# Kernel tuning notes

Measured on AMD Instinct MI355X. Metric: run time of the kernel, lower is better.

## Reference

```python
import jax, jax.numpy as jnp
import numpy as np

HEADS, DIM_HEAD = 8, 64  # per init_kwargs


def cdist(x, w):
    """Euclidean distance between rows of x [..., n, d] and w [m, d] -> [..., n, m].
    Matches torch.cdist (non-squared) / L2DistanceLinear(squared=False)."""
    sq = (x * x).sum(-1, keepdims=True) + (w * w).sum(-1) - 2.0 * (x @ w.T)
    return jnp.sqrt(jnp.maximum(sq, 0.0))


def setup_inputs() -> dict:
    key = jax.random.key(0)
    k1, k2, k3 = jax.random.split(key, 3)
    B, N, D = 4, 2048, 512
    dim_inner = HEADS * DIM_HEAD  # 512
    x = jax.random.normal(k1, (B, N, D), dtype=jnp.float32)
    w_qkv = jax.random.normal(k2, (3 * dim_inner, D), dtype=jnp.float32)
    w_out = jax.random.normal(k3, (D, dim_inner), dtype=jnp.float32)
    return {"x": x, "w_qkv": w_qkv, "w_out": w_out}


def reference(x, w_qkv, w_out):
    B, N, D = x.shape
    scale = DIM_HEAD ** -0.5

    # L2-distance QKV projection (cdist, non-squared, no negate/bias)
    qkv = cdist(x, w_qkv)                                  # [B, N, 3*H*DH]
    qkv = qkv.reshape(B, N, 3, HEADS, DIM_HEAD).transpose(2, 0, 3, 1, 4)  # [3, B, H, N, DH]
    q, k, v = qkv[0], qkv[1], qkv[2]

    # neg squared-L2 attention scores: -(||q||^2 + ||k||^2 - 2 q.k)
    q_sq = (q * q).sum(-1)                                 # [B, H, N]
    k_sq = (k * k).sum(-1)                                 # [B, H, N]
    dots = jnp.einsum('bhid,bhjd->bhij', q, k)             # [B, H, N, N]
    sim = -(q_sq[..., :, None] + k_sq[..., None, :] - 2.0 * dots) * scale

    attn = jax.nn.softmax(sim, axis=-1)
    out = jnp.einsum('bhij,bhjd->bhid', attn, v)           # [B, H, N, DH]
    out = out.transpose(0, 2, 1, 3).reshape(B, N, HEADS * DIM_HEAD)

    # L2-distance output projection
    return cdist(out, w_out)                               # [B, N, D]
```

## Files before the change

### kernel.cpp

```cpp
#include <hip/hip_runtime.h>
#include <stdint.h>

typedef float v4f  __attribute__((ext_vector_type(4)));
typedef float v16f __attribute__((ext_vector_type(16)));
typedef short v8s  __attribute__((ext_vector_type(8)));
typedef uint32_t u32;

#define DEVI static __device__ __forceinline__

DEVI unsigned short f2bf(float f) {
    u32 u = __builtin_bit_cast(u32, f);
    u = (u + 0x7fffu + ((u >> 16) & 1u)) >> 16;
    return (unsigned short)u;
}
DEVI float bf2f(unsigned short h) {
    u32 u = ((u32)h) << 16;
    return __builtin_bit_cast(float, u);
}

template <typename T>
DEVI void async16(const T* g, T* l) {
    __builtin_amdgcn_global_load_lds(
        (const __attribute__((address_space(1))) u32*)g,
        (__attribute__((address_space(3))) u32*)l, 16, 0, 0);
}

DEVI v4f bmfma(v8s a, v8s b, v4f c) {
    return __builtin_amdgcn_mfma_f32_16x16x32_bf16(a, b, c, 0, 0, 0);
}
DEVI v16f bmfma32(v8s a, v8s b, v16f c) {
    return __builtin_amdgcn_mfma_f32_32x32x16_bf16(a, b, c, 0, 0, 0);
}

#if __has_builtin(__builtin_amdgcn_permlane32_swap)
#define HAVE_PLSWAP 1
typedef unsigned int v2u __attribute__((ext_vector_type(2)));
#endif

DEVI void swap32(u32 a, u32 b, u32& lo, u32& hi) {
#ifdef HAVE_PLSWAP
    v2u r = __builtin_amdgcn_permlane32_swap(a, b, false, false);
    lo = r.x; hi = r.y;
#else
    u32 ax = __shfl_xor(a, 32), bx = __shfl_xor(b, 32);
    int hh = (threadIdx.x & 63) >> 5;
    lo = hh ? bx : a;
    hi = hh ? b : ax;
#endif
}

static const size_t HSZ = 32ull * 2048 * 64;

__launch_bounds__(256, 2)
__global__ void prep_all(const float* __restrict__ X, const float* __restrict__ WQ,
                         const float* __restrict__ WO,
                         unsigned short* __restrict__ Xb, unsigned short* __restrict__ WQb,
                         unsigned short* __restrict__ WOb,
                         float* __restrict__ xsq, float* __restrict__ wqsq,
                         float* __restrict__ wosq, float* __restrict__ wors)
{
    const int bid = blockIdx.x;
    const int w = threadIdx.x >> 6, lane = threadIdx.x & 63;
    const float* src; unsigned short* dst; float* Sq; float* Rs = nullptr;
    int r;
    if (bid < 2048)      { src = X;  dst = Xb;  Sq = xsq;  r = bid * 4 + w; }
    else if (bid < 2432) { src = WQ; dst = WQb; Sq = wqsq; r = (bid - 2048) * 4 + w; }
    else                 { src = WO; dst = WOb; Sq = wosq; Rs = wors; r = (bid - 2432) * 4 + w; }

    const float* xr = src + (size_t)r * 512 + lane * 8;
    float4 a = *(const float4*)xr;
    float4 c = *(const float4*)(xr + 4);
    float s = a.x*a.x + a.y*a.y + a.z*a.z + a.w*a.w
            + c.x*c.x + c.y*c.y + c.z*c.z + c.w*c.w;
    float sm = a.x + a.y + a.z + a.w + c.x + c.y + c.z + c.w;
    uint4 pkv;
    unsigned short* e = (unsigned short*)&pkv;
    e[0] = f2bf(a.x); e[1] = f2bf(a.y); e[2] = f2bf(a.z); e[3] = f2bf(a.w);
    e[4] = f2bf(c.x); e[5] = f2bf(c.y); e[6] = f2bf(c.z); e[7] = f2bf(c.w);
    *(uint4*)(dst + (size_t)r * 512 + lane * 8) = pkv;
#pragma unroll
    for (int d = 32; d > 0; d >>= 1) {
        s  += __shfl_xor(s, d);
        sm += __shfl_xor(sm, d);
    }
    if (lane == 0) { Sq[r] = s; if (Rs) Rs[r] = sm; }
}

__launch_bounds__(256, 2)
__global__ void gemm_cdist(const unsigned short* __restrict__ A,
                           const unsigned short* __restrict__ B,
                           const float* __restrict__ Asq,
                           const float* __restrict__ Bsq,
                           unsigned short* __restrict__ QKV,
                           float* __restrict__ Ksqc)
{
    __shared__ unsigned short lsm[2 * 2 * 128 * 32];
    const int t = threadIdx.x;
    const int lane = t & 63, w = t >> 6;
    const int low = lane & 15, quad = lane >> 4;
    const int wm = w & 1, wn = w >> 1;
    const int tM = blockIdx.x * 128, tN = blockIdx.y * 128;

    v4f acc[4][4];
#pragma unroll
    for (int a = 0; a < 4; ++a)
#pragma unroll
        for (int b = 0; b < 4; ++b) acc[a][b] = (v4f){0.f, 0.f, 0.f, 0.f};

    int kstage = 0;
    auto STAGE = [&](int buf) {
        unsigned short* lA = lsm + buf * 8192;
        unsigned short* lB = lA + 4096;
#pragma unroll
        for (int is = 0; is < 2; ++is) {
            int slot = is * 256 + t;
            int r = slot >> 2, bp = slot & 3, bs = bp ^ (r & 3);
            async16(A + (size_t)(tM + r) * 512 + kstage + bs * 8, lA + slot * 8);
            async16(B + (size_t)(tN + r) * 512 + kstage + bs * 8, lB + slot * 8);
        }
        kstage += 32;
    };

    STAGE(0);
    __syncthreads();

#pragma unroll 2
    for (int iter = 0; iter < 16; ++iter) {
        const int c = iter & 1;
        if (iter < 15) STAGE(1 - c);
        const unsigned short* lA = lsm + c * 8192;
        const unsigned short* lB = lA + 4096;

        v8s bfr[4];
#pragma unroll
        for (int ns = 0; ns < 4; ++ns) {
            int row = wn * 64 + ns * 16 + low;
            bfr[ns] = *(const v8s*)(lB + (row * 4 + (quad ^ (row & 3))) * 8);
        }
#pragma unroll
        for (int ms = 0; ms < 4; ++ms) {
            int row = wm * 64 + ms * 16 + low;
            v8s af = *(const v8s*)(lA + (row * 4 + (quad ^ (row & 3))) * 8);
#pragma unroll
            for (int ns = 0; ns < 4; ++ns)
                acc[ms][ns] = bmfma(af, bfr[ns], acc[ms][ns]);
        }
        __syncthreads();
    }

    const int tt = tN >> 9;
    if (tt != 2) {
#pragma unroll
        for (int ms = 0; ms < 4; ++ms) {
#pragma unroll
            for (int reg = 0; reg < 4; ++reg) {
                const int row = tM + wm * 64 + ms * 16 + quad * 4 + reg;
                const int b = row >> 11, i = row & 2047;
                float kacc = 0.f;
#pragma unroll
                for (int ns = 0; ns < 4; ++ns) {
                    const int col = tN + wn * 64 + ns * 16 + low;
                    float dot = acc[ms][ns][reg];
                    float val = sqrtf(fmaxf(Asq[row] + Bsq[col] - 2.f * dot, 0.f)) - 32.f;
                    int h = (col >> 6) & 7, d = col & 63, bh = b * 8 + h;
                    if (tt == 0) {
                        QKV[((size_t)bh * 2048 + i) * 64 + d] =
                            f2bf(val * 0.36067376022224085f);
                    } else {
                        QKV[HSZ + ((size_t)bh * 2048 + i) * 64 + d] = f2bf(val);
                        kacc += val * val;
                    }
                }
                if (tt == 1) {
#pragma unroll
                    for (int d = 1; d < 16; d <<= 1) kacc += __shfl_xor(kacc, d);
                    if (low == 0) {
                        int h = ((tN + wn * 64) >> 6) & 7;
                        Ksqc[(size_t)(b * 8 + h) * 2048 + i] = -kacc * 0.18033688011112042f;
                    }
                }
            }
        }
    } else {
        u32 packed[4][4][2];
#pragma unroll
        for (int ms = 0; ms < 4; ++ms)
#pragma unroll
            for (int ns = 0; ns < 4; ++ns) {
                const int col = tN + wn * 64 + ns * 16 + low;
                float bs_ = Bsq[col];
#pragma unroll
                for (int rp = 0; rp < 2; ++rp) {
                    u32 pk = 0;
#pragma unroll
                    for (int sub = 0; sub < 2; ++sub) {
                        int reg = rp * 2 + sub;
                        int row = tM + wm * 64 + ms * 16 + quad * 4 + reg;
                        float val = sqrtf(fmaxf(Asq[row] + bs_
                                                - 2.f * acc[ms][ns][reg], 0.f)) - 32.f;
                        pk |= (u32)f2bf(val) << (16 * sub);
                    }
                    packed[ms][ns][rp] = pk;
                }
            }
        u32* lT32 = (u32*)lsm;
#pragma unroll
        for (int p = 0; p < 2; ++p) {
            __syncthreads();
            if (wm == p) {
#pragma unroll
                for (int ms = 0; ms < 4; ++ms)
#pragma unroll
                    for (int ns = 0; ns < 4; ++ns) {
                        int cl = wn * 64 + ns * 16 + low;
#pragma unroll
                        for (int rp = 0; rp < 2; ++rp)
                            lT32[cl * 36 + ms * 8 + quad * 2 + rp] = packed[ms][ns][rp];
                    }
            }
            __syncthreads();
#pragma unroll
            for (int cc = 0; cc < 4; ++cc) {
                int col = cc * 32 + (t >> 3);
                int i0 = (t & 7) * 8;
                uint4 vvv = *(const uint4*)(lsm + col * 72 + i0);
                int colg = tN + col;
                int h = (colg >> 6) & 7, d = colg & 63;
                int rowg = tM + p * 64 + i0;
                int b = rowg >> 11, i = rowg & 2047;
                *(uint4*)(QKV + 2 * HSZ
                          + ((size_t)((b * 8 + h) * 64 + d)) * 2048 + i) = vvv;
            }
        }
    }
    (void)0;
}

__launch_bounds__(256, 2)
__global__ void flash_attn(const unsigned short* __restrict__ Q,
                           const unsigned short* __restrict__ K,
                           const unsigned short* __restrict__ VT,
                           const float* __restrict__ Ksqc,
                           unsigned short* __restrict__ PO,
                           float* __restrict__ PL)
{
    __shared__ unsigned short lK[2][64 * 64];
    __shared__ unsigned short lV[2][64 * 64];
    __shared__ float lKq[2][64];
    const int t = threadIdx.x, lane = t & 63, w = t >> 6;
    const int i31 = lane & 31, h = lane >> 5;
    const int qt = blockIdx.x, bh = blockIdx.y, sp = blockIdx.z;
    const size_t base = (size_t)bh * (2048 * 64);
    const int row0 = qt * 128 + w * 32;
    const int j0 = sp * 1024;

    v8s qfr[4];
#pragma unroll
    for (int kt = 0; kt < 4; ++kt)
        qfr[kt] = *(const v8s*)(Q + base + (size_t)(row0 + i31) * 64 + kt * 16 + h * 8);

    v16f o[2];
    float lacc = 0.f;
#pragma unroll
    for (int dt = 0; dt < 2; ++dt)
#pragma unroll
        for (int r = 0; r < 16; ++r) o[dt][r] = 0.f;

    const unsigned short* kg = K + base + (size_t)j0 * 64;
    const unsigned short* vg = VT + (size_t)bh * 64 * 2048 + j0;
    const float* kqg = Ksqc + (size_t)bh * 2048 + j0;

    auto STAGE = [&](int buf) {
#pragma unroll
        for (int is = 0; is < 2; ++is) {
            int slot = is * 256 + t;
            int r = slot >> 3, bp = slot & 7, bs = bp ^ (r & 7);
            async16(kg + (size_t)r * 64 + bs * 8, &lK[buf][slot * 8]);
        }
#pragma unroll
        for (int is = 0; is < 2; ++is) {
            int slot = is * 256 + t;
            int r = slot >> 3, bp = slot & 7, bs = bp ^ (r & 7);
            async16(vg + (size_t)r * 2048 + bs * 8, &lV[buf][slot * 8]);
        }
        if (t < 16) async16(kqg + t * 4, &lKq[buf][t * 4]);
        kg += 64 * 64; vg += 64; kqg += 64;
    };

    STAGE(0);
    __syncthreads();

#pragma unroll 2
    for (int iter = 0; iter < 16; ++iter) {
        const int c = iter & 1;
        if (iter < 15) STAGE(1 - c);

#pragma unroll
        for (int T = 0; T < 2; ++T) {
            const int jrow = T * 32 + i31;
            v8s kf[4];
#pragma unroll
            for (int kt = 0; kt < 4; ++kt)
                kf[kt] = *(const v8s*)(&lK[c][(jrow * 8 + ((2 * kt + h) ^ (jrow & 7))) * 8]);

            v16f sa;
#pragma unroll
            for (int r1 = 0; r1 < 4; ++r1) {
                v4f kq = *(const v4f*)(&lKq[c][T * 32 + r1 * 8 + h * 4]);
#pragma unroll
                for (int u = 0; u < 4; ++u) sa[4 * r1 + u] = kq[u];
            }
            __builtin_amdgcn_s_setprio(1);
#pragma unroll
            for (int kt = 0; kt < 4; ++kt)
                sa = bmfma32(kf[kt], qfr[kt], sa);
            u32 pk[8];
#pragma unroll
            for (int r1 = 0; r1 < 4; ++r1) {
                float p0 = exp2f(sa[4 * r1 + 0]);
                float p1 = exp2f(sa[4 * r1 + 1]);
                float p2 = exp2f(sa[4 * r1 + 2]);
                float p3 = exp2f(sa[4 * r1 + 3]);
                lacc += (p0 + p1) + (p2 + p3);
                pk[2 * r1] = __builtin_amdgcn_perm(
                    __builtin_bit_cast(u32, p1), __builtin_bit_cast(u32, p0),
                    0x07060302u);
                pk[2 * r1 + 1] = __builtin_amdgcn_perm(
                    __builtin_bit_cast(u32, p3), __builtin_bit_cast(u32, p2),
                    0x07060302u);
            }
#pragma unroll
            for (int c2 = 0; c2 < 2; ++c2) {
                const int jb = 2 * (2 * T + c2);
                v8s vf[2];
#pragma unroll
                for (int dt = 0; dt < 2; ++dt) {
                    const int drow = dt * 32 + i31;
                    vf[dt] = *(const v8s*)(&lV[c][(drow * 8 + ((jb + h) ^ (drow & 7))) * 8]);
                }
                uint4 dd;
                swap32(pk[4 * c2 + 0], pk[4 * c2 + 2], dd.x, dd.z);
                swap32(pk[4 * c2 + 1], pk[4 * c2 + 3], dd.y, dd.w);
                v8s af = __builtin_bit_cast(v8s, dd);
                o[0] = bmfma32(af, vf[0], o[0]);
                o[1] = bmfma32(af, vf[1], o[1]);
            }
            __builtin_amdgcn_s_setprio(0);
        }
        __syncthreads();
    }

    const int pb = (qt * 32 + bh) * 2 + sp;
    unsigned short* pob = PO + (size_t)pb * 8192;
    lacc += __shfl_xor(lacc, 32);
#pragma unroll
    for (int dt = 0; dt < 2; ++dt)
#pragma unroll
        for (int r = 0; r < 16; ++r) {
            int rl = w * 32 + (r & 3) + 8 * (r >> 2) + 4 * h;
            pob[rl * 64 + dt * 32 + i31] = f2bf(o[dt][r]);
        }
    if (h == 0)
        PL[(size_t)pb * 128 + w * 32 + i31] = lacc;
}

__launch_bounds__(256, 2)
__global__ void combine_kernel(const unsigned short* __restrict__ PO,
                               const float* __restrict__ PL,
                               unsigned short* __restrict__ O,
                               float* __restrict__ Osqp)
{
    const int qt = blockIdx.x, bh = blockIdx.y, t = threadIdx.x;
    const int b = bh >> 3, h = bh & 7;
    const int pbase = ((qt >> 1) * 32 + bh) * 2;
    const int rl = (qt & 1) * 64 + (t >> 2), c0 = (t & 3) * 16;
    float inv = 1.f / (PL[(size_t)pbase * 128 + rl] + PL[(size_t)(pbase + 1) * 128 + rl]);
    const unsigned short* a = PO + (size_t)pbase * 8192 + rl * 64 + c0;
    const unsigned short* bb = a + 8192;
    uint4 a0 = *(const uint4*)a,  a1 = *(const uint4*)(a + 8);
    uint4 b0 = *(const uint4*)bb, b1 = *(const uint4*)(bb + 8);
    const unsigned short* ae = (const unsigned short*)&a0;
    const unsigned short* be = (const unsigned short*)&b0;
    uint4 o0, o1;
    unsigned short* oe = (unsigned short*)&o0;
#pragma unroll
    for (int u = 0; u < 8; ++u) oe[u] = f2bf((bf2f(ae[u]) + bf2f(be[u])) * inv);
    ae = (const unsigned short*)&a1; be = (const unsigned short*)&b1;
    oe = (unsigned short*)&o1;
#pragma unroll
    for (int u = 0; u < 8; ++u) oe[u] = f2bf((bf2f(ae[u]) + bf2f(be[u])) * inv);
    unsigned short* dst = O + ((size_t)(b * 2048 + qt * 64 + (t >> 2))) * 512 + h * 64 + c0;
    *(uint4*)dst = o0;
    *(uint4*)(dst + 8) = o1;

    const unsigned short* q0 = (const unsigned short*)&o0;
    const unsigned short* q1 = (const unsigned short*)&o1;
    float s = 0.f;
#pragma unroll
    for (int u = 0; u < 8; ++u) { float f = bf2f(q0[u]) + 32.f; s += f * f; }
#pragma unroll
    for (int u = 0; u < 8; ++u) { float f = bf2f(q1[u]) + 32.f; s += f * f; }
    s += __shfl_xor(s, 1);
    s += __shfl_xor(s, 2);
    if ((t & 3) == 0)
        Osqp[(size_t)h * 8192 + b * 2048 + qt * 64 + (t >> 2)] = s;
}

__launch_bounds__(256, 2)
__global__ void gemm_out(const unsigned short* __restrict__ A,
                         const unsigned short* __restrict__ B,
                         const float* __restrict__ Osqp,
                         const float* __restrict__ Bsq,
                         const float* __restrict__ Brs,
                         float* __restrict__ OUT)
{
    __shared__ unsigned short lA[2][128 * 64];
    __shared__ unsigned short lB[2][64 * 64];
    __shared__ float lAsq[128];
    const int t = threadIdx.x;
    const int lane = t & 63, w = t >> 6;
    const int low = lane & 15, quad = lane >> 4;
    const int wm = w & 1, wn = w >> 1;
    const int tM = blockIdx.x * 128, tN = blockIdx.y * 64;

    if (t < 128) {
        float s = 0.f;
#pragma unroll
        for (int hh = 0; hh < 8; ++hh) s += Osqp[(size_t)hh * 8192 + tM + t];
        lAsq[t] = s;
    }

    v4f acc[4][2];
#pragma unroll
    for (int a = 0; a < 4; ++a)
#pragma unroll
        for (int b = 0; b < 2; ++b) acc[a][b] = (v4f){0.f, 0.f, 0.f, 0.f};

    int kstage = 0;
    auto STAGE = [&](int buf) {
#pragma unroll
        for (int is = 0; is < 4; ++is) {
            int slot = is * 256 + t;
            int r = slot >> 3, bp = slot & 7, bs = bp ^ (r & 7);
            async16(A + (size_t)(tM + r) * 512 + kstage + bs * 8, &lA[buf][slot * 8]);
        }
#pragma unroll
        for (int is = 0; is < 2; ++is) {
            int slot = is * 256 + t;
            int r = slot >> 3, bp = slot & 7, bs = bp ^ (r & 7);
            async16(B + (size_t)(tN + r) * 512 + kstage + bs * 8, &lB[buf][slot * 8]);
        }
        kstage += 64;
    };

    STAGE(0);
    __syncthreads();

#pragma unroll 2
    for (int iter = 0; iter < 8; ++iter) {
        const int c = iter & 1;
        if (iter < 7) STAGE(1 - c);

        v8s bfr[2][2];
#pragma unroll
        for (int ns = 0; ns < 2; ++ns) {
            int row = wn * 32 + ns * 16 + low;
#pragma unroll
            for (int kc = 0; kc < 2; ++kc)
                bfr[ns][kc] = *(const v8s*)(&lB[c][(row * 8 + ((kc * 4 + quad) ^ (row & 7))) * 8]);
        }
#pragma unroll
        for (int ms = 0; ms < 4; ++ms) {
            int row = wm * 64 + ms * 16 + low;
            v8s af0 = *(const v8s*)(&lA[c][(row * 8 + ((0 + quad) ^ (row & 7))) * 8]);
            v8s af1 = *(const v8s*)(&lA[c][(row * 8 + ((4 + quad) ^ (row & 7))) * 8]);
#pragma unroll
            for (int ns = 0; ns < 2; ++ns) {
                acc[ms][ns] = bmfma(af0, bfr[ns][0], acc[ms][ns]);
                acc[ms][ns] = bmfma(af1, bfr[ns][1], acc[ms][ns]);
            }
        }
        __syncthreads();
    }

#pragma unroll
    for (int ms = 0; ms < 4; ++ms) {
#pragma unroll
        for (int ns = 0; ns < 2; ++ns) {
#pragma unroll
            for (int reg = 0; reg < 4; ++reg) {
                int rloc = wm * 64 + ms * 16 + quad * 4 + reg;
                int row = tM + rloc;
                int col = tN + wn * 32 + ns * 16 + low;
                float val = sqrtf(fmaxf(lAsq[rloc] + Bsq[col]
                                        - 2.f * (acc[ms][ns][reg] + 32.f * Brs[col]), 0.f));
                OUT[(size_t)row * 512 + col] = val;
            }
        }
    }
}

extern "C" void kernel_launch(void* const* d_in, const int* in_sizes, int n_in,
                              void* d_out, int out_size, void* d_ws, size_t ws_size,
                              hipStream_t stream)
{
    const float* x    = (const float*)d_in[0];
    const float* wqkv = (const float*)d_in[1];
    const float* wout = (const float*)d_in[2];
    float* out = (float*)d_out;

    char* ws = (char*)d_ws;
    size_t off = 0;
    auto alloc = [&](size_t bytes) -> void* {
        void* p = ws + off;
        off += (bytes + 255) & ~(size_t)255;
        return p;
    };
    unsigned short* xb   = (unsigned short*)alloc(8192ull * 512 * 2);
    unsigned short* wqb  = (unsigned short*)alloc(1536ull * 512 * 2);
    unsigned short* wob  = (unsigned short*)alloc(512ull * 512 * 2);
    unsigned short* qkv  = (unsigned short*)alloc(3ull * HSZ * 2);
    unsigned short* outp = (unsigned short*)alloc(8192ull * 512 * 2);
    unsigned short* po   = (unsigned short*)alloc(1024ull * 8192 * 2);
    float* pl   = (float*)alloc(1024ull * 128 * 4);
    float* xsq  = (float*)alloc(8192 * 4);
    float* wqsq = (float*)alloc(1536 * 4);
    float* wosq = (float*)alloc(512 * 4);
    float* wors = (float*)alloc(512 * 4);
    float* ksqc = (float*)alloc(65536ull * 4);
    float* osqp = (float*)alloc(8ull * 8192 * 4);

    prep_all<<<2560, 256, 0, stream>>>(x, wqkv, wout, xb, wqb, wob,
                                       xsq, wqsq, wosq, wors);

    gemm_cdist<<<dim3(64, 12), 256, 0, stream>>>(xb, wqb, xsq, wqsq, qkv, ksqc);
    flash_attn<<<dim3(16, 32, 2), 256, 0, stream>>>(qkv, qkv + HSZ, qkv + 2 * HSZ,
                                                    ksqc, po, pl);
    combine_kernel<<<dim3(32, 32), 256, 0, stream>>>(po, pl, outp, osqp);
    gemm_out<<<dim3(64, 8), 256, 0, stream>>>(outp, wob, osqp, wosq, wors, out);
}
```

Baseline: 174.8 us.

## Drop split-KV in flash attention and fuse normalization into epilogue

Flash attention now runs each query tile over the full key range in one block instead of splitting across two blocks, and normalizes, writes the bf16 output and computes the per-row squared norms directly in its epilogue. This removes the combine kernel launch and the partial-output round trip through global memory. In exchange the grid halves to 512 blocks, each doing twice the loop iterations, which may lower occupancy and parallelism on a large GPU. The s_setprio hints around the MFMA section are also removed.

New measurement: 171.9 us. About the same (-1.6%).

```diff
diff --git a/kernel.cpp b/kernel.cpp
--- a/kernel.cpp
+++ b/kernel.cpp
@@ -241,18 +241,17 @@
                            const unsigned short* __restrict__ K,
                            const unsigned short* __restrict__ VT,
                            const float* __restrict__ Ksqc,
-                           unsigned short* __restrict__ PO,
-                           float* __restrict__ PL)
+                           unsigned short* __restrict__ OP,
+                           float* __restrict__ Osqp)
 {
     __shared__ unsigned short lK[2][64 * 64];
     __shared__ unsigned short lV[2][64 * 64];
     __shared__ float lKq[2][64];
     const int t = threadIdx.x, lane = t & 63, w = t >> 6;
     const int i31 = lane & 31, h = lane >> 5;
-    const int qt = blockIdx.x, bh = blockIdx.y, sp = blockIdx.z;
+    const int qt = blockIdx.x, bh = blockIdx.y;
     const size_t base = (size_t)bh * (2048 * 64);
     const int row0 = qt * 128 + w * 32;
-    const int j0 = sp * 1024;
 
     v8s qfr[4];
 #pragma unroll
@@ -266,9 +265,9 @@
 #pragma unroll
         for (int r = 0; r < 16; ++r) o[dt][r] = 0.f;
 
-    const unsigned short* kg = K + base + (size_t)j0 * 64;
-    const unsigned short* vg = VT + (size_t)bh * 64 * 2048 + j0;
-    const float* kqg = Ksqc + (size_t)bh * 2048 + j0;
+    const unsigned short* kg = K + base;
+    const unsigned short* vg = VT + (size_t)bh * 64 * 2048;
+    const float* kqg = Ksqc + (size_t)bh * 2048;
 
     auto STAGE = [&](int buf) {
 #pragma unroll
@@ -291,9 +290,9 @@
     __syncthreads();
 
 #pragma unroll 2
-    for (int iter = 0; iter < 16; ++iter) {
+    for (int iter = 0; iter < 32; ++iter) {
         const int c = iter & 1;
-        if (iter < 15) STAGE(1 - c);
+        if (iter < 31) STAGE(1 - c);
 
 #pragma unroll
         for (int T = 0; T < 2; ++T) {
@@ -310,7 +309,6 @@
 #pragma unroll
                 for (int u = 0; u < 4; ++u) sa[4 * r1 + u] = kq[u];
             }
-            __builtin_amdgcn_s_setprio(1);
 #pragma unroll
             for (int kt = 0; kt < 4; ++kt)
                 sa = bmfma32(kf[kt], qfr[kt], sa);
@@ -345,65 +343,28 @@
                 o[0] = bmfma32(af, vf[0], o[0]);
                 o[1] = bmfma32(af, vf[1], o[1]);
             }
-            __builtin_amdgcn_s_setprio(0);
         }
         __syncthreads();
     }
 
-    const int pb = (qt * 32 + bh) * 2 + sp;
-    unsigned short* pob = PO + (size_t)pb * 8192;
+    const int b = bh >> 3, hh = bh & 7;
     lacc += __shfl_xor(lacc, 32);
-#pragma unroll
-    for (int dt = 0; dt < 2; ++dt)
-#pragma unroll
-        for (int r = 0; r < 16; ++r) {
-            int rl = w * 32 + (r & 3) + 8 * (r >> 2) + 4 * h;
-            pob[rl * 64 + dt * 32 + i31] = f2bf(o[dt][r]);
-        }
-    if (h == 0)
-        PL[(size_t)pb * 128 + w * 32 + i31] = lacc;
-}
-
-__launch_bounds__(256, 2)
-__global__ void combine_kernel(const unsigned short* __restrict__ PO,
-                               const float* __restrict__ PL,
-                               unsigned short* __restrict__ O,
-                               float* __restrict__ Osqp)
-{
-    const int qt = blockIdx.x, bh = blockIdx.y, t = threadIdx.x;
-    const int b = bh >> 3, h = bh & 7;
-    const int pbase = ((qt >> 1) * 32 + bh) * 2;
-    const int rl = (qt & 1) * 64 + (t >> 2), c0 = (t & 3) * 16;
-    float inv = 1.f / (PL[(size_t)pbase * 128 + rl] + PL[(size_t)(pbase + 1) * 128 + rl]);
-    const unsigned short* a = PO + (size_t)pbase * 8192 + rl * 64 + c0;
-    const unsigned short* bb = a + 8192;
-    uint4 a0 = *(const uint4*)a,  a1 = *(const uint4*)(a + 8);
-    uint4 b0 = *(const uint4*)bb, b1 = *(const uint4*)(bb + 8);
-    const unsigned short* ae = (const unsigned short*)&a0;
-    const unsigned short* be = (const unsigned short*)&b0;
-    uint4 o0, o1;
-    unsigned short* oe = (unsigned short*)&o0;
-#pragma unroll
-    for (int u = 0; u < 8; ++u) oe[u] = f2bf((bf2f(ae[u]) + bf2f(be[u])) * inv);
-    ae = (const unsigned short*)&a1; be = (const unsigned short*)&b1;
-    oe = (unsigned short*)&o1;
-#pragma unroll
-    for (int u = 0; u < 8; ++u) oe[u] = f2bf((bf2f(ae[u]) + bf2f(be[u])) * inv);
-    unsigned short* dst = O + ((size_t)(b * 2048 + qt * 64 + (t >> 2))) * 512 + h * 64 + c0;
-    *(uint4*)dst = o0;
-    *(uint4*)(dst + 8) = o1;
-
-    const unsigned short* q0 = (const unsigned short*)&o0;
-    const unsigned short* q1 = (const unsigned short*)&o1;
-    float s = 0.f;
-#pragma unroll
-    for (int u = 0; u < 8; ++u) { float f = bf2f(q0[u]) + 32.f; s += f * f; }
-#pragma unroll
-    for (int u = 0; u < 8; ++u) { float f = bf2f(q1[u]) + 32.f; s += f * f; }
-    s += __shfl_xor(s, 1);
-    s += __shfl_xor(s, 2);
-    if ((t & 3) == 0)
-        Osqp[(size_t)h * 8192 + b * 2048 + qt * 64 + (t >> 2)] = s;
+    unsigned short* ob = OP + ((size_t)(b * 2048 + row0)) * 512 + hh * 64;
+    float* osq = Osqp + (size_t)hh * 8192 + b * 2048 + row0;
+#pragma unroll
+    for (int r = 0; r < 16; ++r) {
+        const int rl = (r & 3) + 8 * (r >> 2) + 4 * h;
+        float inv = 1.f / __shfl(lacc, rl);
+        unsigned short e0 = f2bf(o[0][r] * inv);
+        unsigned short e1 = f2bf(o[1][r] * inv);
+        ob[(size_t)rl * 512 + i31] = e0;
+        ob[(size_t)rl * 512 + 32 + i31] = e1;
+        float f0 = bf2f(e0) + 32.f, f1 = bf2f(e1) + 32.f;
+        float s = f0 * f0 + f1 * f1;
+        s += __shfl_xor(s, 1);  s += __shfl_xor(s, 2);  s += __shfl_xor(s, 4);
+        s += __shfl_xor(s, 8);  s += __shfl_xor(s, 16);
+        if (i31 == 0) osq[rl] = s;
+    }
 }
 
 __launch_bounds__(256, 2)
@@ -521,8 +482,6 @@
     unsigned short* wob  = (unsigned short*)alloc(512ull * 512 * 2);
     unsigned short* qkv  = (unsigned short*)alloc(3ull * HSZ * 2);
     unsigned short* outp = (unsigned short*)alloc(8192ull * 512 * 2);
-    unsigned short* po   = (unsigned short*)alloc(1024ull * 8192 * 2);
-    float* pl   = (float*)alloc(1024ull * 128 * 4);
     float* xsq  = (float*)alloc(8192 * 4);
     float* wqsq = (float*)alloc(1536 * 4);
     float* wosq = (float*)alloc(512 * 4);
@@ -534,8 +493,7 @@
                                        xsq, wqsq, wosq, wors);
 
     gemm_cdist<<<dim3(64, 12), 256, 0, stream>>>(xb, wqb, xsq, wqsq, qkv, ksqc);
-    flash_attn<<<dim3(16, 32, 2), 256, 0, stream>>>(qkv, qkv + HSZ, qkv + 2 * HSZ,
-                                                    ksqc, po, pl);
-    combine_kernel<<<dim3(32, 32), 256, 0, stream>>>(po, pl, outp, osqp);
+    flash_attn<<<dim3(16, 32), 256, 0, stream>>>(qkv, qkv + HSZ, qkv + 2 * HSZ,
+                                                 ksqc, outp, osqp);
     gemm_out<<<dim3(64, 8), 256, 0, stream>>>(outp, wob, osqp, wosq, wors, out);
 }
```
